# Kernel optimization log

Hardware: AMD Instinct MI355X
Metric: run time of the kernel (lower is better)

The kernel has to match this reference:

```python
import jax, jax.numpy as jnp
import numpy as np

N = 100000        # nodes
E = 3200000       # edges
IN = 256          # in_feats
H = 8             # num_heads
O = 64            # out_feats
F = 64            # edge_feats
T = 8             # num_etypes

def setup_inputs() -> dict:
    key = jax.random.key(0)
    ks = jax.random.split(key, 10)
    return {
        "feat": jax.random.normal(ks[0], (N, IN), jnp.float32) * 0.1,
        "etype": jax.random.randint(ks[1], (E,), 0, T, jnp.int32),
        "src": jax.random.randint(ks[2], (E,), 0, N, jnp.int32),
        "dst": jax.random.randint(ks[3], (E,), 0, N, jnp.int32),
        "W_fc": jax.random.normal(ks[4], (IN, H * O), jnp.float32) * (1.0 / np.sqrt(IN)),
        "edge_emb": jax.random.normal(ks[5], (T, F), jnp.float32),
        "W_e": jax.random.normal(ks[6], (F, H * F), jnp.float32) * (1.0 / np.sqrt(F)),
        "attn_l": jax.random.normal(ks[7], (H, O), jnp.float32) * 0.1,
        "attn_r": jax.random.normal(ks[8], (H, O), jnp.float32) * 0.1,
        "attn_e": jax.random.normal(ks[9], (H, F), jnp.float32) * 0.1,
    }

def reference(feat, etype, src, dst, W_fc, edge_emb, W_e, attn_l, attn_r, attn_e):
    n = feat.shape[0]
    # node projection + per-head attention logits
    h = (feat @ W_fc).reshape(n, H, O)                      # [N,H,O]
    el = jnp.einsum('nho,ho->nh', h, attn_l)                # [N,H]
    er = jnp.einsum('nho,ho->nh', h, attn_r)                # [N,H]
    # edge-type embedding -> projection -> logit (project the tiny table once, then gather)
    emb_proj = (edge_emb @ W_e).reshape(T, H, F)            # [T,H,F]
    ee = jnp.einsum('thf,hf->th', emb_proj, attn_e)[etype]  # [E,H]
    # u_add_v + edge bias, then ReLU (module's "leaky_relu" is nn.ReLU())
    e = jax.nn.relu(el[src] + er[dst] + ee)                 # [E,H]
    # segment softmax grouped by destination node
    m = jax.ops.segment_max(e, dst, num_segments=n)         # [N,H]
    ex = jnp.exp(e - m[dst])                                # [E,H]
    s = jax.ops.segment_sum(ex, dst, num_segments=n)        # [N,H]
    return ex / s[dst]                                      # [E,H]
```

## Files before the change

kernel.cpp:

```cpp
#include <hip/hip_runtime.h>
#include <math.h>

#define NN 100000
#define NE 3200000
#define INF_ 256
#define NH 8
#define OF 64
#define EF 64
#define NT 8

#define BSH 7
#define BNODES 128
#define NB 782
#define SPLIT 4
#define EPB 4096

typedef unsigned long long u64;

static constexpr size_t WS_AT     = 0;
static constexpr size_t WS_EE     = 4096;
static constexpr size_t WS_EL     = 4160;
static constexpr size_t WS_ERS    = WS_EL + (size_t)NN * 8;
static constexpr size_t WS_CCNT   = WS_ERS + (size_t)NN * 16;
static constexpr size_t WS_BASE   = WS_CCNT + NB;
static constexpr size_t WS_CUR    = WS_BASE + NB + 1;
static constexpr size_t WS_PART64 = ((WS_CUR + NB + 1) & ~(size_t)1);

__global__ __launch_bounds__(256) void k_prep_A(const float* __restrict__ W_fc,
                                                const float* __restrict__ attn_l,
                                                const float* __restrict__ attn_r,
                                                float* __restrict__ At,
                                                unsigned* __restrict__ ccnt) {
    int t = blockIdx.x * 256 + threadIdx.x;
    if (t < NB) ccnt[t] = 0u;
    int c = t >> 8;
    int i = t & 255;
    int h = c & 7;
    const float* attn = (c < 8) ? attn_l : attn_r;
    const float* wrow = W_fc + (size_t)i * (NH * OF) + h * OF;
    const float* arow = attn + h * OF;
    float acc = 0.f;
#pragma unroll 8
    for (int o = 0; o < OF; ++o) acc += wrow[o] * arow[o];
    At[c * INF_ + i] = acc;
}

__global__ __launch_bounds__(512) void k_prep_ee(const float* __restrict__ edge_emb,
                                                 const float* __restrict__ W_e,
                                                 const float* __restrict__ attn_e,
                                                 float* __restrict__ ee_tab) {
    __shared__ float B[EF][NH];
    int t = threadIdx.x;
    int g = t >> 3, h = t & 7;
    const float* wrow = W_e + (size_t)g * (NH * EF) + h * EF;
    const float* arow = attn_e + h * EF;
    float acc = 0.f;
#pragma unroll 8
    for (int f = 0; f < EF; ++f) acc += wrow[f] * arow[f];
    B[g][h] = acc;
    __syncthreads();
    if (t < NT * NH) {
        int tt = t >> 3, hh = t & 7;
        float a = 0.f;
#pragma unroll 8
        for (int g2 = 0; g2 < EF; ++g2) a += edge_emb[tt * EF + g2] * B[g2][hh];
        ee_tab[tt * NH + hh] = a;
    }
}

__global__ __launch_bounds__(256) void k_node(const float* __restrict__ feat,
                                              const float* __restrict__ At,
                                              float* __restrict__ el,
                                              float* __restrict__ ers) {
    int n = blockIdx.x * 256 + threadIdx.x;
    if (n >= NN) return;
    const float4* f4 = (const float4*)(feat + (size_t)n * INF_);
    const float4* A4 = (const float4*)At;
    float acc[16];
#pragma unroll
    for (int c = 0; c < 16; ++c) acc[c] = 0.f;
    for (int iq = 0; iq < INF_ / 4; ++iq) {
        float4 f = f4[iq];
#pragma unroll
        for (int c = 0; c < 16; ++c) {
            float4 a = A4[c * 64 + iq];
            acc[c] += f.x * a.x + f.y * a.y + f.z * a.z + f.w * a.w;
        }
    }
    float4* e4 = (float4*)(el + (size_t)n * 8);
    e4[0] = make_float4(acc[0], acc[1], acc[2], acc[3]);
    e4[1] = make_float4(acc[4], acc[5], acc[6], acc[7]);
    float4* r4 = (float4*)(ers + (size_t)n * 16);
    r4[0] = make_float4(acc[8], acc[9], acc[10], acc[11]);
    r4[1] = make_float4(acc[12], acc[13], acc[14], acc[15]);
    r4[2] = make_float4(0.f, 0.f, 0.f, 0.f);
    r4[3] = make_float4(0.f, 0.f, 0.f, 0.f);
}

__global__ __launch_bounds__(256) void k_count(const int* __restrict__ dst,
                                               unsigned* __restrict__ ccnt) {
    __shared__ unsigned hist[NB];
    int tid = threadIdx.x;
    size_t base = (size_t)blockIdx.x * EPB;
    for (int i = tid; i < NB; i += 256) hist[i] = 0u;
    __syncthreads();
#pragma unroll
    for (int k = 0; k < 16; ++k) {
        size_t j = base + (size_t)k * 256 + tid;
        if (j < NE) atomicAdd(&hist[dst[j] >> BSH], 1u);
    }
    __syncthreads();
    for (int i = tid; i < NB; i += 256) {
        unsigned h = hist[i];
        if (h) atomicAdd(ccnt + i, h);
    }
}

__global__ __launch_bounds__(256) void k_scan(const unsigned* __restrict__ ccnt,
                                              unsigned* __restrict__ base,
                                              unsigned* __restrict__ cur) {
    __shared__ unsigned v[NB];
    int t = threadIdx.x;
    for (int i = t; i < NB; i += 256) v[i] = ccnt[i];
    __syncthreads();
    if (t == 0) {
        unsigned acc = 0;
        for (int i = 0; i < NB; ++i) { unsigned c = v[i]; v[i] = acc; acc += c; }
    }
    __syncthreads();
    for (int i = t; i < NB; i += 256) { base[i] = v[i]; cur[i] = v[i]; }
    if (t == 0) base[NB] = NE;
}

__global__ __launch_bounds__(256) void k_partition(const int* __restrict__ src,
                                                   const int* __restrict__ dst,
                                                   const int* __restrict__ etype,
                                                   unsigned* __restrict__ cur,
                                                   u64* __restrict__ part64) {
    __shared__ unsigned hist[NB];
    __shared__ unsigned curs[NB];
    int tid = threadIdx.x;
    size_t base = (size_t)blockIdx.x * EPB;
    u64 rc[16];
    for (int i = tid; i < NB; i += 256) hist[i] = 0u;
    __syncthreads();
#pragma unroll
    for (int k = 0; k < 16; ++k) {
        size_t j = base + (size_t)k * 256 + tid;
        if (j < NE) {
            int dj = dst[j];
            rc[k] = (u64)(unsigned)src[j]
                  | ((u64)(unsigned)etype[j] << 17)
                  | ((u64)(unsigned)dj << 20);
            atomicAdd(&hist[dj >> BSH], 1u);
        } else rc[k] = ~0ull;
    }
    __syncthreads();
    for (int i = tid; i < NB; i += 256) {
        unsigned h = hist[i];
        curs[i] = h ? atomicAdd(cur + i, h) : 0u;
    }
    __syncthreads();
#pragma unroll
    for (int k = 0; k < 16; ++k) {
        if (rc[k] == ~0ull) continue;
        int dj = (int)(rc[k] >> 20);
        int b = dj >> BSH;
        unsigned pos = atomicAdd(&curs[b], 1u);
        unsigned eid = (unsigned)(base + (size_t)k * 256 + tid);
        part64[pos] = (rc[k] & 0xFFFFFull)
                    | ((u64)(unsigned)(dj & (BNODES - 1)) << 20)
                    | ((u64)eid << 27);
    }
}

__global__ __launch_bounds__(256) void k_bucket_sum(const u64* __restrict__ part64,
                                                    const unsigned* __restrict__ base,
                                                    const float* __restrict__ el,
                                                    const float* __restrict__ ers,
                                                    const float* __restrict__ ee_tab,
                                                    float* __restrict__ ers_out) {
    __shared__ float sbin[BNODES * 9];
    __shared__ float er_l[BNODES * 9];
    __shared__ float ee_l[NT * NH];
    int bs = blockIdx.x;
    int b = bs >> 2, c = bs & 3;
    int tid = threadIdx.x;
    int n0 = b << BSH;
    int nn = NN - n0; if (nn > BNODES) nn = BNODES;

    for (int i = tid; i < BNODES * 9; i += 256) sbin[i] = 0.f;
    if (tid < NT * NH) ee_l[tid] = ee_tab[tid];
    for (int i = tid; i < nn * NH; i += 256) {
        int nl = i >> 3, hh = i & 7;
        er_l[nl * 9 + hh] = ers[(size_t)(n0 + nl) * 16 + hh];
    }
    __syncthreads();

    unsigned lo = base[b], hiB = base[b + 1];
    for (unsigned e = lo + (unsigned)(c * 256 + tid); e < hiB; e += 1024) {
        u64 rec = part64[e];
        int sj = (int)(rec & 0x1FFFFu);
        int et = (int)((rec >> 17) & 7u);
        int dl = (int)((rec >> 20) & (BNODES - 1));
        const float4* el4 = (const float4*)(el + (size_t)sj * 8);
        float4 la = el4[0], lb = el4[1];
        const float* erp = &er_l[dl * 9];
        const float* eep = &ee_l[et * 8];
        float* sb = &sbin[dl * 9];
        atomicAdd(&sb[0], __expf(fmaxf(la.x + erp[0] + eep[0], 0.f)));
        atomicAdd(&sb[1], __expf(fmaxf(la.y + erp[1] + eep[1], 0.f)));
        atomicAdd(&sb[2], __expf(fmaxf(la.z + erp[2] + eep[2], 0.f)));
        atomicAdd(&sb[3], __expf(fmaxf(la.w + erp[3] + eep[3], 0.f)));
        atomicAdd(&sb[4], __expf(fmaxf(lb.x + erp[4] + eep[4], 0.f)));
        atomicAdd(&sb[5], __expf(fmaxf(lb.y + erp[5] + eep[5], 0.f)));
        atomicAdd(&sb[6], __expf(fmaxf(lb.z + erp[6] + eep[6], 0.f)));
        atomicAdd(&sb[7], __expf(fmaxf(lb.w + erp[7] + eep[7], 0.f)));
    }
    __syncthreads();
    for (int i = tid; i < nn * NH; i += 256) {
        int nl = i >> 3, hh = i & 7;
        atomicAdd(&ers_out[(size_t)(n0 + nl) * 16 + 8 + hh], sbin[nl * 9 + hh]);
    }
}

__global__ __launch_bounds__(256) void k_out(const u64* __restrict__ part64,
                                             const unsigned* __restrict__ base,
                                             const float* __restrict__ el,
                                             const float* __restrict__ ers,
                                             const float* __restrict__ ee_tab,
                                             float* __restrict__ out) {
    __shared__ float st[BNODES * 17];
    __shared__ float ee_l[NT * NH];
    int bs = blockIdx.x;
    int b = bs >> 2, c = bs & 3;
    int tid = threadIdx.x;
    int n0 = b << BSH;
    int nn = NN - n0; if (nn > BNODES) nn = BNODES;

    if (tid < NT * NH) ee_l[tid] = ee_tab[tid];
    for (int i = tid; i < nn * 16; i += 256) {
        int nl = i >> 4, q = i & 15;
        float v = ers[(size_t)(n0 + nl) * 16 + q];
        st[nl * 17 + q] = (q < 8) ? v : 1.0f / v;
    }
    __syncthreads();

    unsigned lo = base[b], hiB = base[b + 1];
    for (unsigned e = lo + (unsigned)(c * 256 + tid); e < hiB; e += 1024) {
        u64 rec = part64[e];
        int sj = (int)(rec & 0x1FFFFu);
        int et = (int)((rec >> 17) & 7u);
        int dl = (int)((rec >> 20) & (BNODES - 1));
        unsigned eid = (unsigned)(rec >> 27);
        const float4* el4 = (const float4*)(el + (size_t)sj * 8);
        float4 la = el4[0], lb = el4[1];
        const float* sp = &st[dl * 17];
        const float* eep = &ee_l[et * 8];
        float4 o0, o1;
        o0.x = __expf(fmaxf(la.x + sp[0] + eep[0], 0.f)) * sp[8];
        o0.y = __expf(fmaxf(la.y + sp[1] + eep[1], 0.f)) * sp[9];
        o0.z = __expf(fmaxf(la.z + sp[2] + eep[2], 0.f)) * sp[10];
        o0.w = __expf(fmaxf(la.w + sp[3] + eep[3], 0.f)) * sp[11];
        o1.x = __expf(fmaxf(lb.x + sp[4] + eep[4], 0.f)) * sp[12];
        o1.y = __expf(fmaxf(lb.y + sp[5] + eep[5], 0.f)) * sp[13];
        o1.z = __expf(fmaxf(lb.z + sp[6] + eep[6], 0.f)) * sp[14];
        o1.w = __expf(fmaxf(lb.w + sp[7] + eep[7], 0.f)) * sp[15];
        float4* o4 = (float4*)(out + (size_t)eid * 8);
        o4[0] = o0;
        o4[1] = o1;
    }
}

extern "C" void kernel_launch(void* const* d_in, const int* in_sizes, int n_in,
                              void* d_out, int out_size, void* d_ws, size_t ws_size,
                              hipStream_t stream) {
    const float* feat     = (const float*)d_in[0];
    const int*   etype    = (const int*)d_in[1];
    const int*   src      = (const int*)d_in[2];
    const int*   dst      = (const int*)d_in[3];
    const float* W_fc     = (const float*)d_in[4];
    const float* edge_emb = (const float*)d_in[5];
    const float* W_e      = (const float*)d_in[6];
    const float* attn_l   = (const float*)d_in[7];
    const float* attn_r   = (const float*)d_in[8];
    const float* attn_e   = (const float*)d_in[9];

    float*    ws      = (float*)d_ws;
    float*    At      = ws + WS_AT;
    float*    ee_tab  = ws + WS_EE;
    float*    el      = ws + WS_EL;
    float*    ers     = ws + WS_ERS;
    unsigned* ccnt    = (unsigned*)(ws + WS_CCNT);
    unsigned* basep   = (unsigned*)(ws + WS_BASE);
    unsigned* cur     = (unsigned*)(ws + WS_CUR);
    u64*      part64  = (u64*)(ws + WS_PART64);
    float*    out     = (float*)d_out;

    hipLaunchKernelGGL(k_prep_A, dim3(16), dim3(256), 0, stream, W_fc, attn_l, attn_r, At, ccnt);
    hipLaunchKernelGGL(k_prep_ee, dim3(1), dim3(512), 0, stream, edge_emb, W_e, attn_e, ee_tab);
    hipLaunchKernelGGL(k_node, dim3((NN + 255) / 256), dim3(256), 0, stream, feat, At, el, ers);
    hipLaunchKernelGGL(k_count, dim3((NE + EPB - 1) / EPB), dim3(256), 0, stream, dst, ccnt);
    hipLaunchKernelGGL(k_scan, dim3(1), dim3(256), 0, stream, ccnt, basep, cur);
    hipLaunchKernelGGL(k_partition, dim3((NE + EPB - 1) / EPB), dim3(256), 0, stream,
                       src, dst, etype, cur, part64);
    hipLaunchKernelGGL(k_bucket_sum, dim3(NB * SPLIT), dim3(256), 0, stream,
                       part64, basep, el, ers, ee_tab, ers);
    hipLaunchKernelGGL(k_out, dim3(NB * SPLIT), dim3(256), 0, stream,
                       part64, basep, el, ers, ee_tab, out);
}
```

Before: 594.0 us.

## Fuse bucket softmax-sum and output passes into one per-bucket kernel

Merges the denominator-accumulation kernel and the output kernel into a single kernel, one block per 64-node bucket. Each thread keeps up to ten edge records and their exp values in registers, so the second pass reuses them instead of re-reading part64 and el and recomputing exp. The per-node sums stay in shared memory, which removes the global atomics and the padded ers buffer. Output writes use nontemporal stores. The cost is higher register pressure, fewer blocks, and a slower fallback loop for buckets with more edges than fit in registers.

After: 689.4 us. 16.1% more time.

```diff
diff --git a/kernel.cpp b/kernel.cpp
--- a/kernel.cpp
+++ b/kernel.cpp
@@ -9,19 +9,20 @@
 #define EF 64
 #define NT 8
 
-#define BSH 7
-#define BNODES 128
-#define NB 782
-#define SPLIT 4
+#define BSH 6
+#define BNODES 64
+#define NB 1563
 #define EPB 4096
+#define MAXI 10
 
 typedef unsigned long long u64;
+typedef float vf4 __attribute__((ext_vector_type(4)));
 
 static constexpr size_t WS_AT     = 0;
 static constexpr size_t WS_EE     = 4096;
 static constexpr size_t WS_EL     = 4160;
-static constexpr size_t WS_ERS    = WS_EL + (size_t)NN * 8;
-static constexpr size_t WS_CCNT   = WS_ERS + (size_t)NN * 16;
+static constexpr size_t WS_ER     = WS_EL + (size_t)NN * 8;
+static constexpr size_t WS_CCNT   = WS_ER + (size_t)NN * 8;
 static constexpr size_t WS_BASE   = WS_CCNT + NB;
 static constexpr size_t WS_CUR    = WS_BASE + NB + 1;
 static constexpr size_t WS_PART64 = ((WS_CUR + NB + 1) & ~(size_t)1);
@@ -71,7 +72,7 @@
 __global__ __launch_bounds__(256) void k_node(const float* __restrict__ feat,
                                               const float* __restrict__ At,
                                               float* __restrict__ el,
-                                              float* __restrict__ ers) {
+                                              float* __restrict__ er) {
     int n = blockIdx.x * 256 + threadIdx.x;
     if (n >= NN) return;
     const float4* f4 = (const float4*)(feat + (size_t)n * INF_);
@@ -90,11 +91,9 @@
     float4* e4 = (float4*)(el + (size_t)n * 8);
     e4[0] = make_float4(acc[0], acc[1], acc[2], acc[3]);
     e4[1] = make_float4(acc[4], acc[5], acc[6], acc[7]);
-    float4* r4 = (float4*)(ers + (size_t)n * 16);
+    float4* r4 = (float4*)(er + (size_t)n * 8);
     r4[0] = make_float4(acc[8], acc[9], acc[10], acc[11]);
     r4[1] = make_float4(acc[12], acc[13], acc[14], acc[15]);
-    r4[2] = make_float4(0.f, 0.f, 0.f, 0.f);
-    r4[3] = make_float4(0.f, 0.f, 0.f, 0.f);
 }
 
 __global__ __launch_bounds__(256) void k_count(const int* __restrict__ dst,
@@ -170,21 +169,20 @@
         unsigned eid = (unsigned)(base + (size_t)k * 256 + tid);
         part64[pos] = (rc[k] & 0xFFFFFull)
                     | ((u64)(unsigned)(dj & (BNODES - 1)) << 20)
-                    | ((u64)eid << 27);
-    }
-}
-
-__global__ __launch_bounds__(256) void k_bucket_sum(const u64* __restrict__ part64,
-                                                    const unsigned* __restrict__ base,
-                                                    const float* __restrict__ el,
-                                                    const float* __restrict__ ers,
-                                                    const float* __restrict__ ee_tab,
-                                                    float* __restrict__ ers_out) {
+                    | ((u64)eid << 26);
+    }
+}
+
+__global__ __launch_bounds__(256) void k_fused(const u64* __restrict__ part64,
+                                               const unsigned* __restrict__ base,
+                                               const float* __restrict__ el,
+                                               const float* __restrict__ er,
+                                               const float* __restrict__ ee_tab,
+                                               float* __restrict__ out) {
     __shared__ float sbin[BNODES * 9];
     __shared__ float er_l[BNODES * 9];
     __shared__ float ee_l[NT * NH];
-    int bs = blockIdx.x;
-    int b = bs >> 2, c = bs & 3;
+    int b = blockIdx.x;
     int tid = threadIdx.x;
     int n0 = b << BSH;
     int nn = NN - n0; if (nn > BNODES) nn = BNODES;
@@ -193,12 +191,50 @@
     if (tid < NT * NH) ee_l[tid] = ee_tab[tid];
     for (int i = tid; i < nn * NH; i += 256) {
         int nl = i >> 3, hh = i & 7;
-        er_l[nl * 9 + hh] = ers[(size_t)(n0 + nl) * 16 + hh];
+        er_l[nl * 9 + hh] = er[(size_t)(n0 + nl) * 8 + hh];
     }
     __syncthreads();
 
     unsigned lo = base[b], hiB = base[b + 1];
-    for (unsigned e = lo + (unsigned)(c * 256 + tid); e < hiB; e += 1024) {
+    u64 rc[MAXI];
+    float4 exA[MAXI], exB[MAXI];
+
+#pragma unroll
+    for (int k = 0; k < MAXI; ++k) {
+        unsigned e = lo + (unsigned)(k * 256 + tid);
+        rc[k] = (e < hiB) ? __builtin_nontemporal_load(part64 + e) : ~0ull;
+    }
+#pragma unroll
+    for (int k = 0; k < MAXI; ++k) {
+        if (rc[k] != ~0ull) {
+            int sj = (int)(rc[k] & 0x1FFFFu);
+            int et = (int)((rc[k] >> 17) & 7u);
+            int dl = (int)((rc[k] >> 20) & (BNODES - 1));
+            const float4* el4 = (const float4*)(el + (size_t)sj * 8);
+            float4 la = el4[0], lb = el4[1];
+            const float* erp = &er_l[dl * 9];
+            const float* eep = &ee_l[et * 8];
+            float4 a, bq;
+            a.x = __expf(fmaxf(la.x + erp[0] + eep[0], 0.f));
+            a.y = __expf(fmaxf(la.y + erp[1] + eep[1], 0.f));
+            a.z = __expf(fmaxf(la.z + erp[2] + eep[2], 0.f));
+            a.w = __expf(fmaxf(la.w + erp[3] + eep[3], 0.f));
+            bq.x = __expf(fmaxf(lb.x + erp[4] + eep[4], 0.f));
+            bq.y = __expf(fmaxf(lb.y + erp[5] + eep[5], 0.f));
+            bq.z = __expf(fmaxf(lb.z + erp[6] + eep[6], 0.f));
+            bq.w = __expf(fmaxf(lb.w + erp[7] + eep[7], 0.f));
+            exA[k] = a; exB[k] = bq;
+            float* sb = &sbin[dl * 9];
+            atomicAdd(&sb[0], a.x);  atomicAdd(&sb[1], a.y);
+            atomicAdd(&sb[2], a.z);  atomicAdd(&sb[3], a.w);
+            atomicAdd(&sb[4], bq.x); atomicAdd(&sb[5], bq.y);
+            atomicAdd(&sb[6], bq.z); atomicAdd(&sb[7], bq.w);
+        } else {
+            exA[k] = make_float4(0.f, 0.f, 0.f, 0.f);
+            exB[k] = make_float4(0.f, 0.f, 0.f, 0.f);
+        }
+    }
+    for (unsigned e = lo + (unsigned)(MAXI * 256 + tid); e < hiB; e += 256) {
         u64 rec = part64[e];
         int sj = (int)(rec & 0x1FFFFu);
         int et = (int)((rec >> 17) & 7u);
@@ -220,55 +256,48 @@
     __syncthreads();
     for (int i = tid; i < nn * NH; i += 256) {
         int nl = i >> 3, hh = i & 7;
-        atomicAdd(&ers_out[(size_t)(n0 + nl) * 16 + 8 + hh], sbin[nl * 9 + hh]);
-    }
-}
-
-__global__ __launch_bounds__(256) void k_out(const u64* __restrict__ part64,
-                                             const unsigned* __restrict__ base,
-                                             const float* __restrict__ el,
-                                             const float* __restrict__ ers,
-                                             const float* __restrict__ ee_tab,
-                                             float* __restrict__ out) {
-    __shared__ float st[BNODES * 17];
-    __shared__ float ee_l[NT * NH];
-    int bs = blockIdx.x;
-    int b = bs >> 2, c = bs & 3;
-    int tid = threadIdx.x;
-    int n0 = b << BSH;
-    int nn = NN - n0; if (nn > BNODES) nn = BNODES;
-
-    if (tid < NT * NH) ee_l[tid] = ee_tab[tid];
-    for (int i = tid; i < nn * 16; i += 256) {
-        int nl = i >> 4, q = i & 15;
-        float v = ers[(size_t)(n0 + nl) * 16 + q];
-        st[nl * 17 + q] = (q < 8) ? v : 1.0f / v;
-    }
-    __syncthreads();
-
-    unsigned lo = base[b], hiB = base[b + 1];
-    for (unsigned e = lo + (unsigned)(c * 256 + tid); e < hiB; e += 1024) {
+        sbin[nl * 9 + hh] = 1.0f / sbin[nl * 9 + hh];
+    }
+    __syncthreads();
+#pragma unroll
+    for (int k = 0; k < MAXI; ++k) {
+        if (rc[k] != ~0ull) {
+            int dl = (int)((rc[k] >> 20) & (BNODES - 1));
+            unsigned eid = (unsigned)(rc[k] >> 26);
+            const float* sp = &sbin[dl * 9];
+            vf4 o0, o1;
+            o0.x = exA[k].x * sp[0]; o0.y = exA[k].y * sp[1];
+            o0.z = exA[k].z * sp[2]; o0.w = exA[k].w * sp[3];
+            o1.x = exB[k].x * sp[4]; o1.y = exB[k].y * sp[5];
+            o1.z = exB[k].z * sp[6]; o1.w = exB[k].w * sp[7];
+            vf4* o4 = (vf4*)(out + (size_t)eid * 8);
+            __builtin_nontemporal_store(o0, o4);
+            __builtin_nontemporal_store(o1, o4 + 1);
+        }
+    }
+    for (unsigned e = lo + (unsigned)(MAXI * 256 + tid); e < hiB; e += 256) {
         u64 rec = part64[e];
         int sj = (int)(rec & 0x1FFFFu);
         int et = (int)((rec >> 17) & 7u);
         int dl = (int)((rec >> 20) & (BNODES - 1));
-        unsigned eid = (unsigned)(rec >> 27);
+        unsigned eid = (unsigned)(rec >> 26);
         const float4* el4 = (const float4*)(el + (size_t)sj * 8);
         float4 la = el4[0], lb = el4[1];
-        const float* sp = &st[dl * 17];
+        const float* erp = &er_l[dl * 9];
         const float* eep = &ee_l[et * 8];
-        float4 o0, o1;
-        o0.x = __expf(fmaxf(la.x + sp[0] + eep[0], 0.f)) * sp[8];
-        o0.y = __expf(fmaxf(la.y + sp[1] + eep[1], 0.f)) * sp[9];
-        o0.z = __expf(fmaxf(la.z + sp[2] + eep[2], 0.f)) * sp[10];
-        o0.w = __expf(fmaxf(la.w + sp[3] + eep[3], 0.f)) * sp[11];
-        o1.x = __expf(fmaxf(lb.x + sp[4] + eep[4], 0.f)) * sp[12];
-        o1.y = __expf(fmaxf(lb.y + sp[5] + eep[5], 0.f)) * sp[13];
-        o1.z = __expf(fmaxf(lb.z + sp[6] + eep[6], 0.f)) * sp[14];
-        o1.w = __expf(fmaxf(lb.w + sp[7] + eep[7], 0.f)) * sp[15];
-        float4* o4 = (float4*)(out + (size_t)eid * 8);
-        o4[0] = o0;
-        o4[1] = o1;
+        const float* sp = &sbin[dl * 9];
+        vf4 o0, o1;
+        o0.x = __expf(fmaxf(la.x + erp[0] + eep[0], 0.f)) * sp[0];
+        o0.y = __expf(fmaxf(la.y + erp[1] + eep[1], 0.f)) * sp[1];
+        o0.z = __expf(fmaxf(la.z + erp[2] + eep[2], 0.f)) * sp[2];
+        o0.w = __expf(fmaxf(la.w + erp[3] + eep[3], 0.f)) * sp[3];
+        o1.x = __expf(fmaxf(lb.x + erp[4] + eep[4], 0.f)) * sp[4];
+        o1.y = __expf(fmaxf(lb.y + erp[5] + eep[5], 0.f)) * sp[5];
+        o1.z = __expf(fmaxf(lb.z + erp[6] + eep[6], 0.f)) * sp[6];
+        o1.w = __expf(fmaxf(lb.w + erp[7] + eep[7], 0.f)) * sp[7];
+        vf4* o4 = (vf4*)(out + (size_t)eid * 8);
+        __builtin_nontemporal_store(o0, o4);
+        __builtin_nontemporal_store(o1, o4 + 1);
     }
 }
 
@@ -290,7 +319,7 @@
     float*    At      = ws + WS_AT;
     float*    ee_tab  = ws + WS_EE;
     float*    el      = ws + WS_EL;
-    float*    ers     = ws + WS_ERS;
+    float*    er      = ws + WS_ER;
     unsigned* ccnt    = (unsigned*)(ws + WS_CCNT);
     unsigned* basep   = (unsigned*)(ws + WS_BASE);
     unsigned* cur     = (unsigned*)(ws + WS_CUR);
@@ -299,13 +328,11 @@
 
     hipLaunchKernelGGL(k_prep_A, dim3(16), dim3(256), 0, stream, W_fc, attn_l, attn_r, At, ccnt);
     hipLaunchKernelGGL(k_prep_ee, dim3(1), dim3(512), 0, stream, edge_emb, W_e, attn_e, ee_tab);
-    hipLaunchKernelGGL(k_node, dim3((NN + 255) / 256), dim3(256), 0, stream, feat, At, el, ers);
+    hipLaunchKernelGGL(k_node, dim3((NN + 255) / 256), dim3(256), 0, stream, feat, At, el, er);
     hipLaunchKernelGGL(k_count, dim3((NE + EPB - 1) / EPB), dim3(256), 0, stream, dst, ccnt);
     hipLaunchKernelGGL(k_scan, dim3(1), dim3(256), 0, stream, ccnt, basep, cur);
     hipLaunchKernelGGL(k_partition, dim3((NE + EPB - 1) / EPB), dim3(256), 0, stream,
                        src, dst, etype, cur, part64);
-    hipLaunchKernelGGL(k_bucket_sum, dim3(NB * SPLIT), dim3(256), 0, stream,
-                       part64, basep, el, ers, ee_tab, ers);
-    hipLaunchKernelGGL(k_out, dim3(NB * SPLIT), dim3(256), 0, stream,
-                       part64, basep, el, ers, ee_tab, out);
-}
+    hipLaunchKernelGGL(k_fused, dim3(NB), dim3(256), 0, stream,
+                       part64, basep, el, er, ee_tab, out);
+}
```
